# Kernel tuning notes

Hardware: AMD Instinct MI355X
Metric: run time of the kernel (lower is better)

## Reference

```python
import jax, jax.numpy as jnp
import numpy as np

NHEAD = 8
TOP_K = 2


def layernorm(x, g, b, eps=1e-5):
    m = x.mean(-1, keepdims=True)
    v = x.var(-1, keepdims=True)
    return (x - m) * jax.lax.rsqrt(v + eps) * g + b


def causal_conv(x, w, b, dil):
    # x: [N, C, L], w: [O, I, K] (torch layout), left-pad for causality
    pad = (w.shape[-1] - 1) * dil
    y = jax.lax.conv_general_dilated(x, w, (1,), [(pad, 0)], rhs_dilation=(dil,),
                                     dimension_numbers=('NCH', 'OIH', 'NCH'))
    return y + b[None, :, None]


def sinusoidal_pe(L, d):
    pos = jnp.arange(L, dtype=jnp.float32)[:, None]
    div = jnp.exp(jnp.arange(0, d, 2, dtype=jnp.float32) * (-np.log(10000.0) / d))
    pe = jnp.zeros((L, d), jnp.float32)
    pe = pe.at[:, 0::2].set(jnp.sin(pos * div))
    pe = pe.at[:, 1::2].set(jnp.cos(pos * div))
    return pe


def _forward(x, sensor_mask, enc_proj_w, enc_proj_b, tcn_w1, tcn_b1, tcn_w2, tcn_b2,
             enc_norm_g, enc_norm_b, pool_proj_w, pool_proj_b, pos_inter,
             t_wq, t_bq, t_wk, t_bk, t_wv, t_bv, t_wo, t_bo,
             t_ln1_g, t_ln1_b, t_ln2_g, t_ln2_b,
             t_ff1_w, t_ff1_b, t_ff2_w, t_ff2_b, t_out_g, t_out_b,
             exp_w1, exp_b1, exp_w2, exp_b2,
             gate_f_w, gate_f_b, gate_fail_w, gate_fail_b, gate_rca_w, gate_rca_b,
             pred_w, pred_b, fail_w, fail_b, rca_w, rca_b):
    B, L, M = x.shape
    P = enc_proj_w.shape[1]
    D = pool_proj_w.shape[1]
    O = exp_w2.shape[-1]
    # mask sensors, grab last value per sensor (globally standardized)
    xm = jnp.transpose(x, (0, 2, 1)) * sensor_mask[:, :, None]        # [B, M, L]
    last_val = xm[:, :, -1]                                           # [B, M]
    seqs = xm.reshape(B * M, L, 1)
    # per-sensor TCN encoder
    h = seqs @ enc_proj_w + enc_proj_b                                # [BM, L, P]
    h = h + sinusoidal_pe(L, P)[None]
    h = jnp.transpose(h, (0, 2, 1))                                   # [BM, P, L]
    for i in range(tcn_w1.shape[0]):
        dil = 2 ** i
        out = jax.nn.relu(causal_conv(h, tcn_w1[i], tcn_b1[i], dil))
        out = jax.nn.relu(causal_conv(out, tcn_w2[i], tcn_b2[i], dil))
        h = jax.nn.relu(out + h)                                      # channels equal -> identity residual
    h = layernorm(jnp.transpose(h, (0, 2, 1)), enc_norm_g, enc_norm_b)  # [BM, L, T]
    feats = h.reshape(B, M, L, -1) * sensor_mask[:, :, None, None]
    pooled = feats.mean(axis=2)                                       # [B, M, T]
    t = pooled @ pool_proj_w + pool_proj_b                            # [B, M, D]
    # inter-sensor transformer (pre-LN), key padding mask where sensor_mask==0
    t = t + pos_inter[:, :M, :]
    bias = jnp.where(sensor_mask == 0, -1e9, 0.0)[:, None, None, :]   # [B,1,1,M]
    dh = D // NHEAD
    for l in range(t_wq.shape[0]):
        y = layernorm(t, t_ln1_g[l], t_ln1_b[l])
        q = (y @ t_wq[l] + t_bq[l]).reshape(B, M, NHEAD, dh)
        k = (y @ t_wk[l] + t_bk[l]).reshape(B, M, NHEAD, dh)
        v = (y @ t_wv[l] + t_bv[l]).reshape(B, M, NHEAD, dh)
        s = jnp.einsum('bqhd,bkhd->bhqk', q, k) / jnp.sqrt(jnp.float32(dh)) + bias
        a = jax.nn.softmax(s, axis=-1)
        o = jnp.einsum('bhqk,bkhd->bqhd', a, v).reshape(B, M, D) @ t_wo[l] + t_bo[l]
        t = t + o
        y2 = layernorm(t, t_ln2_g[l], t_ln2_b[l])
        t = t + jax.nn.relu(y2 @ t_ff1_w[l] + t_ff1_b[l]) @ t_ff2_w[l] + t_ff2_b[l]
    ctx = layernorm(t, t_out_g, t_out_b) * sensor_mask[:, :, None]    # [B, M, D]
    # global context: masked mean + masked max over valid sensors
    cnt = jnp.maximum(sensor_mask.sum(1, keepdims=True), 1.0)
    mean_ctx = ctx.sum(1) / cnt                                       # [B, D]
    max_ctx = jnp.where(sensor_mask[:, :, None] > 0, ctx, -1e9).max(1)
    g = jnp.concatenate([mean_ctx, max_ctx], -1)                      # [B, 2D]

    def moe(x_exp, gate_in, gw, gb):
        logits = gate_in @ gw + gb                                    # [N, E]
        vals, idx = jax.lax.top_k(logits, TOP_K)
        w = jax.nn.softmax(vals, -1)
        hh = jax.nn.relu(jnp.einsum('nd,edh->neh', x_exp, exp_w1) + exp_b1)
        allo = jnp.einsum('neh,eho->neo', hh, exp_w2) + exp_b2        # [N, E, O]
        sel = jnp.take_along_axis(allo, idx[..., None], axis=1)
        return (sel * w[..., None]).sum(1)                            # [N, O]

    y_f = moe(g, g, gate_f_w, gate_f_b)                               # [B, O]
    y_fail = moe(g, g, gate_fail_w, gate_fail_b)
    tok = ctx.reshape(B * M, D)
    exp_in_rca = jnp.concatenate(
        [tok, jnp.broadcast_to(mean_ctx[:, None, :], (B, M, D)).reshape(B * M, D)], -1)
    y_rca = moe(exp_in_rca, tok, gate_rca_w, gate_rca_b).reshape(B, M, O)
    # heads
    pred_in = jnp.concatenate([pooled, ctx, jnp.broadcast_to(y_f[:, None, :], (B, M, O))], -1)
    pred = pred_in @ pred_w + pred_b + last_val[..., None]            # [B, M, PH]
    fail_out = y_fail @ fail_w + fail_b                               # [B, FH]
    rca_in = jnp.concatenate([pooled, ctx, y_rca], -1)
    rca_out = (rca_in @ rca_w + rca_b)[..., 0]                        # [B, M]
    return jnp.concatenate([pred.reshape(B, -1), fail_out, rca_out], axis=1)


def setup_inputs() -> dict:
    key = jax.random.key(0)
    ks = iter(jax.random.split(key, 64))
    nrm = lambda shape, s=0.05: jax.random.normal(next(ks), shape, jnp.float32) * s
    B, L, M = 16, 512, 32
    P, T, D, E, EH, O = 64, 64, 128, 16, 512, 128
    NL, LEV, K = 2, 4, 3
    return dict(
        x=jax.random.normal(next(ks), (B, L, M), jnp.float32),
        sensor_mask=jax.random.randint(next(ks), (B, M), 0, 2).astype(jnp.float32),
        enc_proj_w=nrm((1, P)), enc_proj_b=jnp.zeros((P,)),
        tcn_w1=nrm((LEV, P, P, K)), tcn_b1=jnp.zeros((LEV, P)),
        tcn_w2=nrm((LEV, P, P, K)), tcn_b2=jnp.zeros((LEV, P)),
        enc_norm_g=jnp.ones((T,)), enc_norm_b=jnp.zeros((T,)),
        pool_proj_w=nrm((T, D)), pool_proj_b=jnp.zeros((D,)),
        pos_inter=nrm((1, M, D), 0.02),
        t_wq=nrm((NL, D, D)), t_bq=jnp.zeros((NL, D)),
        t_wk=nrm((NL, D, D)), t_bk=jnp.zeros((NL, D)),
        t_wv=nrm((NL, D, D)), t_bv=jnp.zeros((NL, D)),
        t_wo=nrm((NL, D, D)), t_bo=jnp.zeros((NL, D)),
        t_ln1_g=jnp.ones((NL, D)), t_ln1_b=jnp.zeros((NL, D)),
        t_ln2_g=jnp.ones((NL, D)), t_ln2_b=jnp.zeros((NL, D)),
        t_ff1_w=nrm((NL, D, 2 * D)), t_ff1_b=jnp.zeros((NL, 2 * D)),
        t_ff2_w=nrm((NL, 2 * D, D)), t_ff2_b=jnp.zeros((NL, D)),
        t_out_g=jnp.ones((D,)), t_out_b=jnp.zeros((D,)),
        exp_w1=nrm((E, 2 * D, EH)), exp_b1=jnp.zeros((E, EH)),
        exp_w2=nrm((E, EH, O)), exp_b2=jnp.zeros((E, O)),
        gate_f_w=nrm((2 * D, E)), gate_f_b=jnp.zeros((E,)),
        gate_fail_w=nrm((2 * D, E)), gate_fail_b=jnp.zeros((E,)),
        gate_rca_w=nrm((D, E)), gate_rca_b=jnp.zeros((E,)),
        pred_w=nrm((T + D + O, 3)), pred_b=jnp.zeros((3,)),
        fail_w=nrm((O, 3)), fail_b=jnp.zeros((3,)),
        rca_w=nrm((T + D + O, 1)), rca_b=jnp.zeros((1,)),
    )


def reference(x, sensor_mask, enc_proj_w, enc_proj_b, tcn_w1, tcn_b1, tcn_w2, tcn_b2,
              enc_norm_g, enc_norm_b, pool_proj_w, pool_proj_b, pos_inter,
              t_wq, t_bq, t_wk, t_bk, t_wv, t_bv, t_wo, t_bo,
              t_ln1_g, t_ln1_b, t_ln2_g, t_ln2_b,
              t_ff1_w, t_ff1_b, t_ff2_w, t_ff2_b, t_out_g, t_out_b,
              exp_w1, exp_b1, exp_w2, exp_b2,
              gate_f_w, gate_f_b, gate_fail_w, gate_fail_b, gate_rca_w, gate_rca_b,
              pred_w, pred_b, fail_w, fail_b, rca_w, rca_b):
    return _forward(x, sensor_mask, enc_proj_w, enc_proj_b, tcn_w1, tcn_b1, tcn_w2, tcn_b2,
                    enc_norm_g, enc_norm_b, pool_proj_w, pool_proj_b, pos_inter,
                    t_wq, t_bq, t_wk, t_bk, t_wv, t_bv, t_wo, t_bo,
                    t_ln1_g, t_ln1_b, t_ln2_g, t_ln2_b,
                    t_ff1_w, t_ff1_b, t_ff2_w, t_ff2_b, t_out_g, t_out_b,
                    exp_w1, exp_b1, exp_w2, exp_b2,
                    gate_f_w, gate_f_b, gate_fail_w, gate_fail_b, gate_rca_w, gate_rca_b,
                    pred_w, pred_b, fail_w, fail_b, rca_w, rca_b)
```

## Files before the change

### kernel.cpp

```cpp
#include <hip/hip_runtime.h>
#include <hip/hip_bf16.h>

#define B_   16
#define L_   512
#define M_   32
#define P_   64
#define D_   128
#define NH_  8
#define NL_  2
#define E_   16
#define EH_  512
#define O_   128

#define CH2   256
#define HALO  60
#define PADF  16
#define ROWS2 336
#define LDW   64

typedef short  bf16x8 __attribute__((ext_vector_type(8)));
typedef float  f32x4  __attribute__((ext_vector_type(4)));
typedef unsigned short us4 __attribute__((ext_vector_type(4)));
typedef unsigned short us8 __attribute__((ext_vector_type(8)));

__device__ __forceinline__ float bf2f(unsigned short h) {
  unsigned u = ((unsigned)h) << 16; float f; __builtin_memcpy(&f, &u, 4); return f;
}
__device__ __forceinline__ unsigned short f2bf(float f) {
  unsigned u; __builtin_memcpy(&u, &f, 4);
  u += 0x7fffu + ((u >> 16) & 1);
  return (unsigned short)(u >> 16);
}
__device__ __forceinline__ int swz(int row, int col_us) {
  return row * LDW + (col_us ^ ((row & 7) << 3));
}

#define XFW_PPW   0
#define XFW_QKVO  8192
#define XFW_F1    139264
#define XFW_F2    204800

__global__ __launch_bounds__(256) void prep_kernel(
    const float* __restrict__ ppw,
    const float* __restrict__ twq, const float* __restrict__ twk,
    const float* __restrict__ twv, const float* __restrict__ two,
    const float* __restrict__ f1w, const float* __restrict__ f2w,
    const float* __restrict__ ew1, const float* __restrict__ ew2,
    const float* __restrict__ tw1, const float* __restrict__ tw2,
    unsigned short* __restrict__ xfw, unsigned short* __restrict__ w1t,
    unsigned short* __restrict__ w2t, unsigned short* __restrict__ wpack,
    float* __restrict__ peT) {
  const int b = blockIdx.x;
  const int tid = threadIdx.x;
  if (b < 834) {
    __shared__ float tl[64][65];
    const float* src; unsigned short* dst; int R, C, tr, tc;
    if (b < 2) {
      src = ppw; dst = xfw + XFW_PPW; R = 64; C = 128; tr = 0; tc = b;
    } else if (b < 34) {
      int t = b - 2; int lg = t >> 2; int l = lg >> 2, gem = lg & 3;
      int tt = t & 3; tr = tt >> 1; tc = tt & 1;
      const float* s4 = (gem == 0) ? twq : (gem == 1) ? twk : (gem == 2) ? twv : two;
      src = s4 + l * 16384; dst = xfw + XFW_QKVO + l * 65536 + gem * 16384; R = 128; C = 128;
    } else if (b < 50) {
      int t = b - 34; int l = t >> 3; int tt = t & 7; tr = tt >> 2; tc = tt & 3;
      src = f1w + l * 32768; dst = xfw + XFW_F1 + l * 32768; R = 128; C = 256;
    } else if (b < 66) {
      int t = b - 50; int l = t >> 3; int tt = t & 7; tr = tt >> 1; tc = tt & 1;
      src = f2w + l * 32768; dst = xfw + XFW_F2 + l * 32768; R = 256; C = 128;
    } else if (b < 578) {
      int t = b - 66; int e = t >> 5; int tt = t & 31; tr = tt >> 3; tc = tt & 7;
      src = ew1 + e * 131072; dst = w1t + e * 131072; R = 256; C = 512;
    } else {
      int t = b - 578; int e = t >> 4; int tt = t & 15; tr = tt >> 1; tc = tt & 1;
      src = ew2 + e * 65536; dst = w2t + e * 65536; R = 512; C = 128;
    }
    for (int i = tid; i < 4096; i += 256) {
      int r = i >> 6, c = i & 63;
      tl[r][c] = src[(tr * 64 + r) * C + tc * 64 + c];
    }
    __syncthreads();
    for (int i = tid; i < 4096; i += 256) {
      int c = i >> 6, r = i & 63;
      dst[(tc * 64 + c) * R + tr * 64 + r] = f2bf(tl[r][c]);
    }
  } else if (b < 840) {
    int base = (b - 834) * 16384;
    for (int q = tid; q < 16384; q += 256) {
      int i = base + q;
      int c = i & 63, o = (i >> 6) & 63, tlc = i >> 12;
      int t = tlc % 3, lc = tlc / 3, lvl = lc >> 1;
      const float* src = (lc & 1) ? tw2 : tw1;
      wpack[i] = f2bf(src[lvl * 12288 + o * 192 + c * 3 + t]);
    }
  } else {
    int base = (b - 840) * 16384;
    for (int q = tid; q < 16384; q += 256) {
      int j = base + q; int ll = j >> 6, c = j & 63;
      float dv = expf(-0.14391157f * (float)(c & ~1));
      float ang = (float)ll * dv;
      peT[j] = (c & 1) ? cosf(ang) : sinf(ang);
    }
  }
}

template <int DIL, bool RES>
__device__ __forceinline__ void conv_mfma(const unsigned short* __restrict__ IN,
                                          unsigned short* __restrict__ OUT,
                                          const unsigned short* __restrict__ Wt,
                                          const float* __restrict__ bias, bool zh) {
  const int tid  = threadIdx.x;
  const int wid  = tid >> 6;
  const int lane = tid & 63;
  const int fr   = lane & 15;
  const int g    = lane >> 4;
  const int ot0  = (wid & 1) * 2;
  const int ng   = wid >> 1;

  bf16x8 Af[2][6];
#pragma unroll
  for (int oo = 0; oo < 2; ++oo)
#pragma unroll
    for (int t = 0; t < 3; ++t)
#pragma unroll
      for (int kh = 0; kh < 2; ++kh) {
        int wr = t * 64 + (ot0 + oo) * 16 + fr;
        Af[oo][t * 2 + kh] = *(const bf16x8*)(Wt + swz(wr, kh * 32 + g * 8));
      }
  float bv[2][4];
#pragma unroll
  for (int oo = 0; oo < 2; ++oo)
#pragma unroll
    for (int j = 0; j < 4; ++j) bv[oo][j] = bias[(ot0 + oo) * 16 + g * 4 + j];

#pragma unroll
  for (int k = 0; k < 3; ++k) {
    const int nt = ng + k * 8;
    if (nt < 20) {
      const int rb = PADF + nt * 16 + fr;
      bf16x8 Bf[6];
#pragma unroll
      for (int t = 0; t < 3; ++t) {
        int r = rb + (t - 2) * DIL;
#pragma unroll
        for (int kh = 0; kh < 2; ++kh)
          Bf[t * 2 + kh] = *(const bf16x8*)(IN + swz(r, kh * 32 + g * 8));
      }
      f32x4 acc[2];
#pragma unroll
      for (int oo = 0; oo < 2; ++oo) {
        f32x4 a; a[0] = bv[oo][0]; a[1] = bv[oo][1]; a[2] = bv[oo][2]; a[3] = bv[oo][3];
        acc[oo] = a;
      }
#pragma unroll
      for (int f = 0; f < 6; ++f)
#pragma unroll
        for (int oo = 0; oo < 2; ++oo)
          acc[oo] = __builtin_amdgcn_mfma_f32_16x16x32_bf16(Af[oo][f], Bf[f], acc[oo], 0, 0, 0);

      const float zm = (zh && rb < PADF + HALO) ? 0.f : 1.f;
#pragma unroll
      for (int oo = 0; oo < 2; ++oo) {
        unsigned short* op = OUT + swz(rb, (ot0 + oo) * 16 + g * 4);
        us4 old;
        if (RES) old = *(const us4*)op;
        us4 st;
#pragma unroll
        for (int j = 0; j < 4; ++j) {
          float v = fmaxf(acc[oo][j], 0.f);
          if (RES) v = fmaxf(v + bf2f(old[j]), 0.f);
          st[j] = f2bf(v * zm);
        }
        *(us4*)op = st;
      }
    }
  }
}

__global__ __launch_bounds__(1024) void tcn_kernel(
    const float* __restrict__ x, const float* __restrict__ mask,
    const float* __restrict__ pw, const float* __restrict__ pb,
    const unsigned short* __restrict__ wpack,
    const float* __restrict__ b1, const float* __restrict__ b2,
    const float* __restrict__ peT,
    const float* __restrict__ lng, const float* __restrict__ lnb,
    float* __restrict__ psum2) {
  extern __shared__ unsigned short smu[];
  unsigned short* A  = smu;
  unsigned short* Bq = A + ROWS2 * LDW;
  unsigned short* W0 = Bq + ROWS2 * LDW;
  unsigned short* W1 = W0 + 192 * LDW;
  float* fbase = (float*)(W1 + 192 * LDW);
  float* xr   = fbase;
  float* pwpb = fbase + 336;
  float* mst  = fbase;
  float* pp   = fbase + 512;

  const int bx = blockIdx.x;
  const int seq = bx & 511;
  const int chunk = bx >> 9;
  const int b = seq >> 5;
  const int m = seq & 31;
  if (mask[b * M_ + m] == 0.0f) return;
  const int tid = threadIdx.x;
  const bool zh = (chunk == 0);
  const int lbase = chunk * CH2 - HALO;

  float4 wreg[2];
#define WLOAD(li)                                                               \
  { wreg[0] = *(const float4*)(wpack + (li) * 12288 + (tid >> 3) * 64 + (tid & 7) * 8); \
    if (tid < 512)                                                              \
      wreg[1] = *(const float4*)(wpack + (li) * 12288 + ((tid >> 3) + 128) * 64 + (tid & 7) * 8); }
#define WSTORE(buf)                                                             \
  { *(float4*)((buf) + swz(tid >> 3, (tid & 7) * 8)) = wreg[0];                 \
    if (tid < 512)                                                              \
      *(float4*)((buf) + swz((tid >> 3) + 128, (tid & 7) * 8)) = wreg[1]; }

  WLOAD(0);
  if (tid < 64)       pwpb[tid] = pw[tid];
  else if (tid < 128) pwpb[tid] = pb[tid - 64];
  if (tid < ROWS2) {
    int w = tid - PADF, l = lbase + w;
    float xv = 0.f;
    if (w >= 0 && w < CH2 + HALO && l >= 0 && l < L_) xv = x[(b * L_ + l) * M_ + m];
    xr[tid] = xv;
  }
  __syncthreads();

  for (int idx = tid; idx < ROWS2 * 8; idx += 1024) {
    int r = idx >> 3, c0 = (idx & 7) * 8;
    int w = r - PADF, l = lbase + w;
    us8 st;
    if (w >= 0 && w < CH2 + HALO && l >= 0 && l < L_) {
      float xv = xr[r];
      const float4* pe4 = (const float4*)(peT + l * 64 + c0);
      float4 pa = pe4[0], pc = pe4[1];
      float pe[8] = {pa.x, pa.y, pa.z, pa.w, pc.x, pc.y, pc.z, pc.w};
#pragma unroll
      for (int j = 0; j < 8; ++j) {
        int c = c0 + j;
        st[j] = f2bf(fmaf(xv, pwpb[c], pwpb[64 + c]) + pe[j]);
      }
    } else {
#pragma unroll
      for (int j = 0; j < 8; ++j) st[j] = 0;
    }
    *(us8*)(A + swz(r, c0)) = st;
  }
  for (int idx = tid; idx < PADF * LDW; idx += 1024) Bq[idx] = 0;
  WSTORE(W0); WLOAD(1);
  __syncthreads();

  conv_mfma<1, false>(A, Bq, W0, b1 + 0,   zh); WSTORE(W1); WLOAD(2); __syncthreads();
  conv_mfma<1, true >(Bq, A, W1, b2 + 0,   zh); WSTORE(W0); WLOAD(3); __syncthreads();
  conv_mfma<2, false>(A, Bq, W0, b1 + 64,  zh); WSTORE(W1); WLOAD(4); __syncthreads();
  conv_mfma<2, true >(Bq, A, W1, b2 + 64,  zh); WSTORE(W0); WLOAD(5); __syncthreads();
  conv_mfma<4, false>(A, Bq, W0, b1 + 128, zh); WSTORE(W1); WLOAD(6); __syncthreads();
  conv_mfma<4, true >(Bq, A, W1, b2 + 128, zh); WSTORE(W0); WLOAD(7); __syncthreads();
  conv_mfma<8, false>(A, Bq, W0, b1 + 192, zh); WSTORE(W1);           __syncthreads();
  conv_mfma<8, true >(Bq, A, W1, b2 + 192, zh);                       __syncthreads();
#undef WLOAD
#undef WSTORE

  if (tid < CH2) {
    int r = PADF + HALO + tid;
    float s = 0.f, ss = 0.f;
#pragma unroll
    for (int c0 = 0; c0 < 64; c0 += 8) {
      bf16x8 vv = *(const bf16x8*)(A + swz(r, c0));
#pragma unroll
      for (int j = 0; j < 8; ++j) { float v = bf2f((unsigned short)vv[j]); s += v; ss += v * v; }
    }
    float mu = s * 0.015625f;
    float var = fmaxf(ss * 0.015625f - mu * mu, 0.0f);
    mst[tid] = mu;
    mst[CH2 + tid] = rsqrtf(var + 1e-5f);
  }
  __syncthreads();
  {
    int p = tid & 63, q = tid >> 6;
    float accp = 0.f;
    int r0 = PADF + HALO + q * 16;
    for (int r = r0; r < r0 + 16; ++r)
      accp += (bf2f(A[swz(r, p)]) - mst[r - PADF - HALO]) * mst[CH2 + r - PADF - HALO];
    pp[tid] = accp;
  }
  __syncthreads();
  if (tid < 64) {
    float acc = 0.f;
#pragma unroll
    for (int q = 0; q < 16; ++q) acc += pp[q * 64 + tid];
    psum2[chunk * 32768 + seq * 64 + tid] = lng[tid] * acc + 256.0f * lnb[tid];
  }
}

__global__ __launch_bounds__(1024) void xf_kernel(
    const float* __restrict__ psum2, const float* __restrict__ mask,
    const unsigned short* __restrict__ xfw,
    const float* __restrict__ ppb, const float* __restrict__ pos,
    const float* __restrict__ bq, const float* __restrict__ bk,
    const float* __restrict__ bv, const float* __restrict__ bo,
    const float* __restrict__ l1g, const float* __restrict__ l1b,
    const float* __restrict__ l2g, const float* __restrict__ l2b,
    const float* __restrict__ f1b, const float* __restrict__ f2b,
    const float* __restrict__ og_, const float* __restrict__ ob_,
    const float* __restrict__ gfw, const float* __restrict__ gfb,
    const float* __restrict__ glw, const float* __restrict__ glb,
    const float* __restrict__ grw, const float* __restrict__ grb,
    float* __restrict__ pooledws, float* __restrict__ ctxws,
    float* __restrict__ gwt, int* __restrict__ ecnt, int* __restrict__ elist,
    unsigned short* __restrict__ xbf) {
  extern __shared__ float sm[];
  float* T    = sm;
  float* QKV  = T + 4224;
  float* S    = QKV + 12672;
  float* gv   = S + 8448;
  float* mkv  = gv + 512;
  unsigned short* Ybf = (unsigned short*)(mkv + 64);
  unsigned short* Yb2 = Ybf + 32 * 136;
  unsigned short* FFH = Yb2 + 32 * 136;
  const int b = blockIdx.x;
  const int tid = threadIdx.x;
  const int wid = tid >> 6;
  const int lane = tid & 63;
  const int fr = lane & 15;
  const int g = lane >> 4;
  const int row32 = tid >> 5;
  const int ln32  = tid & 31;

  if (tid < 32) mkv[tid] = mask[b * 32 + tid];
  for (int idx = tid; idx < 2048; idx += 1024) {
    int mm = idx >> 6, p = idx & 63;
    const float* p4 = psum2 + (b * 32 + mm) * 64 + p;
    float v = (p4[0] + p4[32768]) * mask[b * 32 + mm] * (1.0f / 512.0f);
    pooledws[(b * 32 + mm) * 64 + p] = v;
    Ybf[mm * 136 + p] = f2bf(v);
  }
  __syncthreads();

  {
    int mt = wid >> 3, nt = wid & 7;
    bf16x8 Af[2];
#pragma unroll
    for (int kf = 0; kf < 2; ++kf)
      Af[kf] = *(const bf16x8*)(Ybf + (mt * 16 + fr) * 136 + kf * 32 + g * 8);
    const unsigned short* bp = xfw + XFW_PPW + (nt * 16 + fr) * 64;
    f32x4 acc = {0.f, 0.f, 0.f, 0.f};
#pragma unroll
    for (int kf = 0; kf < 2; ++kf)
      acc = __builtin_amdgcn_mfma_f32_16x16x32_bf16(Af[kf], *(const bf16x8*)(bp + kf * 32 + g * 8), acc, 0, 0, 0);
    int n = nt * 16 + fr;
    float bb = ppb[n];
#pragma unroll
    for (int j = 0; j < 4; ++j) {
      int m = mt * 16 + g * 4 + j;
      T[m * 132 + n] = acc[j] + bb + pos[m * 128 + n];
    }
  }
  __syncthreads();

#define LN_BF(GAMMA, BETA)                                                     \
  {                                                                            \
    int mm = row32, j0 = ln32 * 4;                                             \
    float4 v4 = *(const float4*)(T + mm * 132 + j0);                           \
    float s = v4.x + v4.y + v4.z + v4.w;                                       \
    float ss = v4.x * v4.x + v4.y * v4.y + v4.z * v4.z + v4.w * v4.w;          \
    _Pragma("unroll") for (int mk = 16; mk >= 1; mk >>= 1) {                   \
      s += __shfl_xor(s, mk); ss += __shfl_xor(ss, mk);                        \
    }                                                                          \
    float mu = s * 0.0078125f;                                                 \
    float rstd = rsqrtf(fmaxf(ss * 0.0078125f - mu * mu, 0.f) + 1e-5f);        \
    us4 st;                                                                    \
    float vv[4] = {v4.x, v4.y, v4.z, v4.w};                                    \
    _Pragma("unroll") for (int j = 0; j < 4; ++j)                              \
      st[j] = f2bf((vv[j] - mu) * rstd * (GAMMA)[j0 + j] + (BETA)[j0 + j]);    \
    *(us4*)(Ybf + mm * 136 + j0) = st;                                         \
  }                                                                            \
  __syncthreads();

  for (int l = 0; l < NL_; ++l) {
    LN_BF(l1g + l * 128, l1b + l * 128)
#pragma unroll
    for (int i = 0; i < 3; ++i) {
      int tt = wid * 3 + i;
      int gem = tt >> 4, r = tt & 15, mt = r >> 3, nt = r & 7;
      const unsigned short* wT = xfw + XFW_QKVO + l * 65536 + gem * 16384;
      const float* bias = (gem == 0) ? bq : (gem == 1) ? bk : bv;
      bf16x8 Afr[4];
#pragma unroll
      for (int kf = 0; kf < 4; ++kf)
        Afr[kf] = *(const bf16x8*)(Ybf + (mt * 16 + fr) * 136 + kf * 32 + g * 8);
      const unsigned short* bp = wT + (nt * 16 + fr) * 128;
      f32x4 acc = {0.f, 0.f, 0.f, 0.f};
#pragma unroll
      for (int kf = 0; kf < 4; ++kf)
        acc = __builtin_amdgcn_mfma_f32_16x16x32_bf16(Afr[kf], *(const bf16x8*)(bp + kf * 32 + g * 8), acc, 0, 0, 0);
      int n = nt * 16 + fr;
      float bb = bias[l * 128 + n];
#pragma unroll
      for (int j = 0; j < 4; ++j)
        QKV[(mt * 16 + g * 4 + j) * 396 + gem * 132 + n] = acc[j] + bb;
    }
    __syncthreads();

    {
      int n = ln32;
      float mbias = (mkv[n] == 0.0f) ? -1e9f : 0.f;
#pragma unroll
      for (int t = 0; t < 8; ++t) {
        int task = row32 * 8 + t;
        int h = task >> 5, mm = task & 31;
        const float* qp = QKV + mm * 396 + h * 16;
        const float* kp = QKV + n * 396 + 132 + h * 16;
        float a = 0;
#pragma unroll
        for (int d = 0; d < 16; ++d) a = fmaf(qp[d], kp[d], a);
        a = a * 0.25f + mbias;
        float mx = a;
#pragma unroll
        for (int mk = 16; mk >= 1; mk >>= 1) mx = fmaxf(mx, __shfl_xor(mx, mk));
        float e = __expf(a - mx);
        float sum = e;
#pragma unroll
        for (int mk = 16; mk >= 1; mk >>= 1) sum += __shfl_xor(sum, mk);
        S[h * 1056 + mm * 33 + n] = e / sum;
      }
    }
    __syncthreads();

    {
      int mm = row32, j0 = ln32 * 4, h = j0 >> 4;
      const float* sp = S + h * 1056 + mm * 33;
      f32x4 a = {0.f, 0.f, 0.f, 0.f};
#pragma unroll 8
      for (int n = 0; n < 32; ++n) {
        float p = sp[n];
        float4 v4 = *(const float4*)(QKV + n * 396 + 264 + j0);
        a[0] = fmaf(p, v4.x, a[0]); a[1] = fmaf(p, v4.y, a[1]);
        a[2] = fmaf(p, v4.z, a[2]); a[3] = fmaf(p, v4.w, a[3]);
      }
      us4 st;
#pragma unroll
      for (int j = 0; j < 4; ++j) st[j] = f2bf(a[j]);
      *(us4*)(Yb2 + mm * 136 + j0) = st;
    }
    __syncthreads();

    {
      int mt = wid >> 3, nt = wid & 7;
      bf16x8 Aw[4];
#pragma unroll
      for (int kf = 0; kf < 4; ++kf)
        Aw[kf] = *(const bf16x8*)(Yb2 + (mt * 16 + fr) * 136 + kf * 32 + g * 8);
      const unsigned short* bp = xfw + XFW_QKVO + l * 65536 + 3 * 16384 + (nt * 16 + fr) * 128;
      f32x4 acc = {0.f, 0.f, 0.f, 0.f};
#pragma unroll
      for (int kf = 0; kf < 4; ++kf)
        acc = __builtin_amdgcn_mfma_f32_16x16x32_bf16(Aw[kf], *(const bf16x8*)(bp + kf * 32 + g * 8), acc, 0, 0, 0);
      int n = nt * 16 + fr;
      float bb = bo[l * 128 + n];
#pragma unroll
      for (int j = 0; j < 4; ++j)
        T[(mt * 16 + g * 4 + j) * 132 + n] += acc[j] + bb;
    }
    __syncthreads();

    LN_BF(l2g + l * 128, l2b + l * 128)
#pragma unroll
    for (int i = 0; i < 2; ++i) {
      int tt = wid * 2 + i;
      int mt = tt >> 4, nt = tt & 15;
      bf16x8 Aff[4];
#pragma unroll
      for (int kf = 0; kf < 4; ++kf)
        Aff[kf] = *(const bf16x8*)(Ybf + (mt * 16 + fr) * 136 + kf * 32 + g * 8);
      const unsigned short* bp = xfw + XFW_F1 + l * 32768 + (nt * 16 + fr) * 128;
      f32x4 acc = {0.f, 0.f, 0.f, 0.f};
#pragma unroll
      for (int kf = 0; kf < 4; ++kf)
        acc = __builtin_amdgcn_mfma_f32_16x16x32_bf16(Aff[kf], *(const bf16x8*)(bp + kf * 32 + g * 8), acc, 0, 0, 0);
      int n = nt * 16 + fr;
      float bb = f1b[l * 256 + n];
#pragma unroll
      for (int j = 0; j < 4; ++j)
        FFH[(mt * 16 + g * 4 + j) * 264 + n] = f2bf(fmaxf(acc[j] + bb, 0.f));
    }
    __syncthreads();
    {
      int mt = wid >> 3, nt = wid & 7;
      bf16x8 Af2[8];
#pragma unroll
      for (int kf = 0; kf < 8; ++kf)
        Af2[kf] = *(const bf16x8*)(FFH + (mt * 16 + fr) * 264 + kf * 32 + g * 8);
      const unsigned short* bp = xfw + XFW_F2 + l * 32768 + (nt * 16 + fr) * 256;
      f32x4 acc = {0.f, 0.f, 0.f, 0.f};
#pragma unroll
      for (int kf = 0; kf < 8; ++kf)
        acc = __builtin_amdgcn_mfma_f32_16x16x32_bf16(Af2[kf], *(const bf16x8*)(bp + kf * 32 + g * 8), acc, 0, 0, 0);
      int n = nt * 16 + fr;
      float bb = f2b[l * 128 + n];
#pragma unroll
      for (int j = 0; j < 4; ++j)
        T[(mt * 16 + g * 4 + j) * 132 + n] += acc[j] + bb;
    }
    __syncthreads();
  }
#undef LN_BF

  {
    int mm = row32, j0 = ln32 * 4;
    float4 v4 = *(const float4*)(T + mm * 132 + j0);
    float s = v4.x + v4.y + v4.z + v4.w;
    float ss = v4.x * v4.x + v4.y * v4.y + v4.z * v4.z + v4.w * v4.w;
#pragma unroll
    for (int mk = 16; mk >= 1; mk >>= 1) { s += __shfl_xor(s, mk); ss += __shfl_xor(ss, mk); }
    float mu = s * 0.0078125f;
    float rstd = rsqrtf(fmaxf(ss * 0.0078125f - mu * mu, 0.f) + 1e-5f);
    float mk_ = mkv[mm];
    float vv[4] = {v4.x, v4.y, v4.z, v4.w};
#pragma unroll
    for (int j = 0; j < 4; ++j) {
      float c = ((vv[j] - mu) * rstd * og_[j0 + j] + ob_[j0 + j]) * mk_;
      S[mm * 132 + j0 + j] = c;
      ctxws[(b * 32 + mm) * 128 + j0 + j] = c;
    }
  }
  __syncthreads();
  if (tid < 128) {
    float cnt = 0;
    for (int mm = 0; mm < 32; ++mm) cnt += mkv[mm];
    cnt = fmaxf(cnt, 1.0f);
    float s = 0, mx = -1e9f;
    for (int mm = 0; mm < 32; ++mm) {
      float v = S[mm * 132 + tid];
      s += v;
      if (mkv[mm] > 0.0f) mx = fmaxf(mx, v);
    }
    gv[tid] = s / cnt;
    gv[128 + tid] = mx;
  }
  __syncthreads();

  float* lg = QKV;
  if (tid < 544) {
    int lr = tid >> 4, e = tid & 15;
    float a;
    if (lr == 0) {
      a = gfb[e];
      for (int d = 0; d < 256; ++d) a = fmaf(gv[d], gfw[d * 16 + e], a);
    } else if (lr == 1) {
      a = glb[e];
      for (int d = 0; d < 256; ++d) a = fmaf(gv[d], glw[d * 16 + e], a);
    } else {
      int mm = lr - 2;
      a = grb[e];
      for (int d = 0; d < 128; ++d) a = fmaf(S[mm * 132 + d], grw[d * 16 + e], a);
    }
    lg[lr * 16 + e] = a;
  }
  __syncthreads();
  if (tid < 34) {
    const float* lgr = lg + tid * 16;
    int i0 = 0; float v0 = lgr[0];
    for (int e = 1; e < 16; ++e) if (lgr[e] > v0) { v0 = lgr[e]; i0 = e; }
    int i1 = (i0 == 0) ? 1 : 0; float v1 = lgr[i1];
    for (int e = 0; e < 16; ++e) if (e != i0 && lgr[e] > v1) { v1 = lgr[e]; i1 = e; }
    float e1 = __expf(v1 - v0);
    float w0 = 1.0f / (1.0f + e1);
    int gr = (tid == 0) ? b : (tid == 1) ? (16 + b) : (32 + b * 32 + (tid - 2));
    gwt[2 * gr] = w0;  gwt[2 * gr + 1] = 1.0f - w0;
    int p0 = atomicAdd(&ecnt[i0], 1); elist[i0 * 544 + p0] = 2 * gr;
    int p1 = atomicAdd(&ecnt[i1], 1); elist[i1 * 544 + p1] = 2 * gr + 1;
  }
  for (int j = tid; j < 34 * 256; j += 1024) {
    int lr = j >> 8, d = j & 255;
    float v;
    if (lr < 2) v = gv[d];
    else        v = (d < 128) ? S[(lr - 2) * 132 + d] : gv[d - 128];
    int gr = (lr == 0) ? b : (lr == 1) ? (16 + b) : (32 + b * 32 + (lr - 2));
    xbf[gr * 256 + d] = f2bf(v);
  }
}

__global__ __launch_bounds__(512) void moe_kernel(
    const unsigned short* __restrict__ xbf, const float* __restrict__ gwt,
    const int* __restrict__ elist, const int* __restrict__ ecnt,
    const unsigned short* __restrict__ w1t, const float* __restrict__ eb1,
    const unsigned short* __restrict__ w2t, const float* __restrict__ eb2,
    float* __restrict__ yall) {
  __shared__ unsigned short Xb[16 * 264];
  __shared__ unsigned short Hb[16 * 520];
  __shared__ float wl[16];
  __shared__ int rowl[16];
  const int e = blockIdx.x >> 3;
  const int slot = blockIdx.x & 7;
  const int n = ecnt[e];
  const int ntiles = (n + 15) >> 4;
  const int tid = threadIdx.x;
  const int wid = tid >> 6;
  const int lane = tid & 63;
  const int fr = lane & 15;
  const int g = lane >> 4;

  for (int t = slot; t < ntiles; t += 8) {
    if (tid < 16) {
      int idx = t * 16 + tid;
      int id = (idx < n) ? elist[e * 544 + idx] : -1;
      rowl[tid] = (id >= 0) ? (id >> 1) : -1;
      wl[tid] = (id >= 0) ? gwt[id] : 0.f;
    }
    __syncthreads();
    for (int i = tid; i < 512; i += 512) {
      int r = i >> 5, c8 = (i & 31) * 8;
      int row = rowl[r];
      bf16x8 v = {0, 0, 0, 0, 0, 0, 0, 0};
      if (row >= 0) v = *(const bf16x8*)(xbf + row * 256 + c8);
      *(bf16x8*)(Xb + r * 264 + c8) = v;
    }
    __syncthreads();
    bf16x8 Af[8];
#pragma unroll
    for (int kf = 0; kf < 8; ++kf)
      Af[kf] = *(const bf16x8*)(Xb + fr * 264 + kf * 32 + g * 8);
#pragma unroll
    for (int ntl = 0; ntl < 4; ++ntl) {
      int nt = wid * 4 + ntl;
      const unsigned short* bp = w1t + (e * 512 + nt * 16 + fr) * 256;
      f32x4 acc = {0.f, 0.f, 0.f, 0.f};
#pragma unroll
      for (int kf = 0; kf < 8; ++kf)
        acc = __builtin_amdgcn_mfma_f32_16x16x32_bf16(Af[kf], *(const bf16x8*)(bp + kf * 32 + g * 8), acc, 0, 0, 0);
      int h = nt * 16 + fr;
      float b1v = eb1[e * 512 + h];
#pragma unroll
      for (int j = 0; j < 4; ++j)
        Hb[(g * 4 + j) * 520 + h] = f2bf(fmaxf(acc[j] + b1v, 0.f));
    }
    __syncthreads();
    {
      const unsigned short* bp = w2t + (e * 128 + wid * 16 + fr) * 512;
      f32x4 acc = {0.f, 0.f, 0.f, 0.f};
#pragma unroll
      for (int kf = 0; kf < 16; ++kf) {
        bf16x8 Ah = *(const bf16x8*)(Hb + fr * 520 + kf * 32 + g * 8);
        acc = __builtin_amdgcn_mfma_f32_16x16x32_bf16(Ah, *(const bf16x8*)(bp + kf * 32 + g * 8), acc, 0, 0, 0);
      }
      int o = wid * 16 + fr;
      float b2v = eb2[e * 128 + o];
#pragma unroll
      for (int j = 0; j < 4; ++j) {
        int r = g * 4 + j;
        int row = rowl[r];
        if (row >= 0) atomicAdd(&yall[row * 128 + o], wl[r] * (acc[j] + b2v));
      }
    }
    __syncthreads();
  }
}

__global__ __launch_bounds__(192) void heads_kernel(
    const float* __restrict__ x, const float* __restrict__ mask,
    const float* __restrict__ pooledws, const float* __restrict__ ctxws,
    const float* __restrict__ yf, const float* __restrict__ yfail, const float* __restrict__ yrca,
    const float* __restrict__ pw, const float* __restrict__ pb,
    const float* __restrict__ fw, const float* __restrict__ fb,
    const float* __restrict__ rw, const float* __restrict__ rb,
    float* __restrict__ out) {
  __shared__ float yfb[128];
  int b = blockIdx.x, t = threadIdx.x;
  if (t < 128) yfb[t] = yf[b * 128 + t];
  __syncthreads();
  if (t < 96) {
    int mm = t / 3, o = t - mm * 3;
    int s = b * 32 + mm;
    float a = pb[o];
    const float* pl = pooledws + s * 64;
    for (int i = 0; i < 64; ++i) a = fmaf(pl[i], pw[i * 3 + o], a);
    const float* cx = ctxws + s * 128;
    for (int i = 0; i < 128; ++i) a = fmaf(cx[i], pw[(64 + i) * 3 + o], a);
    for (int i = 0; i < 128; ++i) a = fmaf(yfb[i], pw[(192 + i) * 3 + o], a);
    a += x[(b * 512 + 511) * 32 + mm] * mask[b * 32 + mm];
    out[b * 131 + t] = a;
  } else if (t < 99) {
    int o = t - 96;
    float a = fb[o];
    const float* yl = yfail + b * 128;
    for (int i = 0; i < 128; ++i) a = fmaf(yl[i], fw[i * 3 + o], a);
    out[b * 131 + 96 + o] = a;
  } else if (t < 131) {
    int mm = t - 99;
    int s = b * 32 + mm;
    float a = rb[0];
    const float* pl = pooledws + s * 64;
    for (int i = 0; i < 64; ++i) a = fmaf(pl[i], rw[i], a);
    const float* cx = ctxws + s * 128;
    for (int i = 0; i < 128; ++i) a = fmaf(cx[i], rw[64 + i], a);
    const float* yr = yrca + s * 128;
    for (int i = 0; i < 128; ++i) a = fmaf(yr[i], rw[192 + i], a);
    out[b * 131 + 99 + mm] = a;
  }
}

extern "C" void kernel_launch(void* const* d_in, const int* in_sizes, int n_in,
                              void* d_out, int out_size, void* d_ws, size_t ws_size,
                              hipStream_t stream) {
  (void)in_sizes; (void)n_in; (void)out_size; (void)ws_size;
  const float* x    = (const float*)d_in[0];
  const float* msk  = (const float*)d_in[1];
  const float* epw  = (const float*)d_in[2];
  const float* epb  = (const float*)d_in[3];
  const float* tw1  = (const float*)d_in[4];
  const float* tb1  = (const float*)d_in[5];
  const float* tw2  = (const float*)d_in[6];
  const float* tb2  = (const float*)d_in[7];
  const float* eng  = (const float*)d_in[8];
  const float* enb  = (const float*)d_in[9];
  const float* ppw  = (const float*)d_in[10];
  const float* ppb  = (const float*)d_in[11];
  const float* pos  = (const float*)d_in[12];
  const float* twq  = (const float*)d_in[13];
  const float* tbq  = (const float*)d_in[14];
  const float* twk  = (const float*)d_in[15];
  const float* tbk  = (const float*)d_in[16];
  const float* twv  = (const float*)d_in[17];
  const float* tbv  = (const float*)d_in[18];
  const float* two  = (const float*)d_in[19];
  const float* tbo  = (const float*)d_in[20];
  const float* l1g  = (const float*)d_in[21];
  const float* l1b  = (const float*)d_in[22];
  const float* l2g  = (const float*)d_in[23];
  const float* l2b  = (const float*)d_in[24];
  const float* f1w  = (const float*)d_in[25];
  const float* f1b  = (const float*)d_in[26];
  const float* f2w  = (const float*)d_in[27];
  const float* f2b  = (const float*)d_in[28];
  const float* tog  = (const float*)d_in[29];
  const float* tob  = (const float*)d_in[30];
  const float* ew1  = (const float*)d_in[31];
  const float* eb1  = (const float*)d_in[32];
  const float* ew2  = (const float*)d_in[33];
  const float* eb2  = (const float*)d_in[34];
  const float* gfw  = (const float*)d_in[35];
  const float* gfb  = (const float*)d_in[36];
  const float* glw  = (const float*)d_in[37];
  const float* glb  = (const float*)d_in[38];
  const float* grw  = (const float*)d_in[39];
  const float* grb  = (const float*)d_in[40];
  const float* prw  = (const float*)d_in[41];
  const float* prb  = (const float*)d_in[42];
  const float* fw   = (const float*)d_in[43];
  const float* fb   = (const float*)d_in[44];
  const float* rw   = (const float*)d_in[45];
  const float* rb   = (const float*)d_in[46];

  float* ws      = (float*)d_ws;
  float* psum2   = ws;
  float* pooledw = psum2 + 65536;
  float* ctxw    = pooledw + 32768;
  float* yall    = ctxw + 65536;
  float* gwt     = yall + 69632;
  int*   ecnt    = (int*)(gwt + 1088);
  int*   elist   = ecnt + 16;
  float* peT     = (float*)(elist + 8704);
  unsigned short* wpack = (unsigned short*)(peT + 32768);
  unsigned short* xfw   = wpack + 98304;
  unsigned short* w1t   = xfw + 270336;
  unsigned short* w2t   = w1t + 2097152;
  unsigned short* xbf   = w2t + 1048576;

  const int tcn_lds = (2 * ROWS2 * LDW + 2 * 192 * LDW) * 2 + 1536 * 4;
  const int xf_lds  = (4224 + 12672 + 8448 + 512 + 64) * 4 + (2 * 4352 + 8448) * 2;
  hipFuncSetAttribute((const void*)tcn_kernel, hipFuncAttributeMaxDynamicSharedMemorySize, tcn_lds);
  hipFuncSetAttribute((const void*)xf_kernel,  hipFuncAttributeMaxDynamicSharedMemorySize, xf_lds);

  hipMemsetAsync(yall, 0, 69632 * sizeof(float), stream);
  hipMemsetAsync(ecnt, 0, 16 * sizeof(int), stream);

  prep_kernel<<<842, 256, 0, stream>>>(ppw, twq, twk, twv, two, f1w, f2w, ew1, ew2,
                                       tw1, tw2, xfw, w1t, w2t, wpack, peT);
  tcn_kernel<<<1024, 1024, tcn_lds, stream>>>(x, msk, epw, epb, wpack, tb1, tb2, peT,
                                              eng, enb, psum2);
  xf_kernel<<<16, 1024, xf_lds, stream>>>(psum2, msk, xfw, ppb, pos,
                                          tbq, tbk, tbv, tbo,
                                          l1g, l1b, l2g, l2b, f1b, f2b,
                                          tog, tob,
                                          gfw, gfb, glw, glb, grw, grb,
                                          pooledw, ctxw, gwt, ecnt, elist, xbf);
  moe_kernel<<<128, 512, 0, stream>>>(xbf, gwt, elist, ecnt, w1t, eb1, w2t, eb2, yall);
  heads_kernel<<<16, 192, 0, stream>>>(x, msk, pooledw, ctxw,
                                       yall, yall + 2048, yall + 4096,
                                       prw, prb, fw, fb, rw, rb, (float*)d_out);
}
```

Measured before the change: 241.8 us.

## Process full sequence per block and read conv weights directly from global

The TCN kernel now handles each sensor's whole 512-step sequence in one block, replacing two overlapping 256-step chunks with a 60-row halo. This removes the recomputed halo rows and the half-block of idle row tiles, and the partial-sum merge in the transformer kernel goes away. Conv weights are loaded into registers straight from global memory (L2-cached) instead of being staged through double-buffered LDS, which frees LDS and removes the staging stores. In exchange, the grid halves to 512 blocks, so there is less parallelism across the GPU, and each wave makes global weight loads on every layer.

```diff
diff --git a/kernel.cpp b/kernel.cpp
--- a/kernel.cpp
+++ b/kernel.cpp
@@ -12,10 +12,8 @@
 #define EH_  512
 #define O_   128
 
-#define CH2   256
-#define HALO  60
 #define PADF  16
-#define ROWS2 336
+#define ROWSF 528
 #define LDW   64
 
 typedef short  bf16x8 __attribute__((ext_vector_type(8)));
@@ -105,10 +103,10 @@
 }
 
 template <int DIL, bool RES>
-__device__ __forceinline__ void conv_mfma(const unsigned short* __restrict__ IN,
-                                          unsigned short* __restrict__ OUT,
-                                          const unsigned short* __restrict__ Wt,
-                                          const float* __restrict__ bias, bool zh) {
+__device__ __forceinline__ void conv_gw(const unsigned short* __restrict__ IN,
+                                        unsigned short* __restrict__ OUT,
+                                        const unsigned short* __restrict__ wp,
+                                        const float* __restrict__ bias) {
   const int tid  = threadIdx.x;
   const int wid  = tid >> 6;
   const int lane = tid & 63;
@@ -123,56 +121,51 @@
 #pragma unroll
     for (int t = 0; t < 3; ++t)
 #pragma unroll
-      for (int kh = 0; kh < 2; ++kh) {
-        int wr = t * 64 + (ot0 + oo) * 16 + fr;
-        Af[oo][t * 2 + kh] = *(const bf16x8*)(Wt + swz(wr, kh * 32 + g * 8));
+      for (int kh = 0; kh < 2; ++kh)
+        Af[oo][t * 2 + kh] =
+            *(const bf16x8*)(wp + (t * 64 + (ot0 + oo) * 16 + fr) * 64 + kh * 32 + g * 8);
+  float bv[2][4];
+#pragma unroll
+  for (int oo = 0; oo < 2; ++oo)
+#pragma unroll
+    for (int j = 0; j < 4; ++j) bv[oo][j] = bias[(ot0 + oo) * 16 + g * 4 + j];
+
+#pragma unroll
+  for (int k = 0; k < 4; ++k) {
+    const int rb = PADF + (ng + k * 8) * 16 + fr;
+    bf16x8 Bf[6];
+#pragma unroll
+    for (int t = 0; t < 3; ++t) {
+      int r = rb + (t - 2) * DIL;
+#pragma unroll
+      for (int kh = 0; kh < 2; ++kh)
+        Bf[t * 2 + kh] = *(const bf16x8*)(IN + swz(r, kh * 32 + g * 8));
+    }
+    f32x4 acc[2];
+#pragma unroll
+    for (int oo = 0; oo < 2; ++oo) {
+      f32x4 a; a[0] = bv[oo][0]; a[1] = bv[oo][1]; a[2] = bv[oo][2]; a[3] = bv[oo][3];
+      acc[oo] = a;
+    }
+#pragma unroll
+    for (int f = 0; f < 6; ++f)
+#pragma unroll
+      for (int oo = 0; oo < 2; ++oo)
+        acc[oo] = __builtin_amdgcn_mfma_f32_16x16x32_bf16(Af[oo][f], Bf[f], acc[oo], 0, 0, 0);
+
+#pragma unroll
+    for (int oo = 0; oo < 2; ++oo) {
+      unsigned short* op = OUT + swz(rb, (ot0 + oo) * 16 + g * 4);
+      us4 old;
+      if (RES) old = *(const us4*)op;
+      us4 st;
+#pragma unroll
+      for (int j = 0; j < 4; ++j) {
+        float v = fmaxf(acc[oo][j], 0.f);
+        if (RES) v = fmaxf(v + bf2f(old[j]), 0.f);
+        st[j] = f2bf(v);
       }
-  float bv[2][4];
-#pragma unroll
-  for (int oo = 0; oo < 2; ++oo)
-#pragma unroll
-    for (int j = 0; j < 4; ++j) bv[oo][j] = bias[(ot0 + oo) * 16 + g * 4 + j];
-
-#pragma unroll
-  for (int k = 0; k < 3; ++k) {
-    const int nt = ng + k * 8;
-    if (nt < 20) {
-      const int rb = PADF + nt * 16 + fr;
-      bf16x8 Bf[6];
-#pragma unroll
-      for (int t = 0; t < 3; ++t) {
-        int r = rb + (t - 2) * DIL;
-#pragma unroll
-        for (int kh = 0; kh < 2; ++kh)
-          Bf[t * 2 + kh] = *(const bf16x8*)(IN + swz(r, kh * 32 + g * 8));
-      }
-      f32x4 acc[2];
-#pragma unroll
-      for (int oo = 0; oo < 2; ++oo) {
-        f32x4 a; a[0] = bv[oo][0]; a[1] = bv[oo][1]; a[2] = bv[oo][2]; a[3] = bv[oo][3];
-        acc[oo] = a;
-      }
-#pragma unroll
-      for (int f = 0; f < 6; ++f)
-#pragma unroll
-        for (int oo = 0; oo < 2; ++oo)
-          acc[oo] = __builtin_amdgcn_mfma_f32_16x16x32_bf16(Af[oo][f], Bf[f], acc[oo], 0, 0, 0);
-
-      const float zm = (zh && rb < PADF + HALO) ? 0.f : 1.f;
-#pragma unroll
-      for (int oo = 0; oo < 2; ++oo) {
-        unsigned short* op = OUT + swz(rb, (ot0 + oo) * 16 + g * 4);
-        us4 old;
-        if (RES) old = *(const us4*)op;
-        us4 st;
-#pragma unroll
-        for (int j = 0; j < 4; ++j) {
-          float v = fmaxf(acc[oo][j], 0.f);
-          if (RES) v = fmaxf(v + bf2f(old[j]), 0.f);
-          st[j] = f2bf(v * zm);
-        }
-        *(us4*)op = st;
-      }
+      *(us4*)op = st;
     }
   }
 }
@@ -184,86 +177,64 @@
     const float* __restrict__ b1, const float* __restrict__ b2,
     const float* __restrict__ peT,
     const float* __restrict__ lng, const float* __restrict__ lnb,
-    float* __restrict__ psum2) {
+    float* __restrict__ psum) {
   extern __shared__ unsigned short smu[];
   unsigned short* A  = smu;
-  unsigned short* Bq = A + ROWS2 * LDW;
-  unsigned short* W0 = Bq + ROWS2 * LDW;
-  unsigned short* W1 = W0 + 192 * LDW;
-  float* fbase = (float*)(W1 + 192 * LDW);
-  float* xr   = fbase;
-  float* pwpb = fbase + 336;
-  float* mst  = fbase;
-  float* pp   = fbase + 512;
-
-  const int bx = blockIdx.x;
-  const int seq = bx & 511;
-  const int chunk = bx >> 9;
+  unsigned short* Bq = A + ROWSF * LDW;
+  float* pwpb = (float*)(Bq + ROWSF * LDW);
+  float* mst  = pwpb + 128;
+  float* pp   = mst + 1024;
+
+  const int seq = blockIdx.x;
   const int b = seq >> 5;
   const int m = seq & 31;
   if (mask[b * M_ + m] == 0.0f) return;
   const int tid = threadIdx.x;
-  const bool zh = (chunk == 0);
-  const int lbase = chunk * CH2 - HALO;
-
-  float4 wreg[2];
-#define WLOAD(li)                                                               \
-  { wreg[0] = *(const float4*)(wpack + (li) * 12288 + (tid >> 3) * 64 + (tid & 7) * 8); \
-    if (tid < 512)                                                              \
-      wreg[1] = *(const float4*)(wpack + (li) * 12288 + ((tid >> 3) + 128) * 64 + (tid & 7) * 8); }
-#define WSTORE(buf)                                                             \
-  { *(float4*)((buf) + swz(tid >> 3, (tid & 7) * 8)) = wreg[0];                 \
-    if (tid < 512)                                                              \
-      *(float4*)((buf) + swz((tid >> 3) + 128, (tid & 7) * 8)) = wreg[1]; }
-
-  WLOAD(0);
-  if (tid < 64)       pwpb[tid] = pw[tid];
-  else if (tid < 128) pwpb[tid] = pb[tid - 64];
-  if (tid < ROWS2) {
-    int w = tid - PADF, l = lbase + w;
-    float xv = 0.f;
-    if (w >= 0 && w < CH2 + HALO && l >= 0 && l < L_) xv = x[(b * L_ + l) * M_ + m];
-    xr[tid] = xv;
-  }
-  __syncthreads();
-
-  for (int idx = tid; idx < ROWS2 * 8; idx += 1024) {
-    int r = idx >> 3, c0 = (idx & 7) * 8;
-    int w = r - PADF, l = lbase + w;
-    us8 st;
-    if (w >= 0 && w < CH2 + HALO && l >= 0 && l < L_) {
-      float xv = xr[r];
-      const float4* pe4 = (const float4*)(peT + l * 64 + c0);
-      float4 pa = pe4[0], pc = pe4[1];
-      float pe[8] = {pa.x, pa.y, pa.z, pa.w, pc.x, pc.y, pc.z, pc.w};
-#pragma unroll
-      for (int j = 0; j < 8; ++j) {
-        int c = c0 + j;
-        st[j] = f2bf(fmaf(xv, pwpb[c], pwpb[64 + c]) + pe[j]);
+
+  if (tid < 64)        pwpb[tid] = pw[tid];
+  else if (tid < 128)  pwpb[tid] = pb[tid - 64];
+  __syncthreads();
+
+  if (tid < ROWSF) {
+    int r = tid;
+    if (r >= PADF) {
+      int l = r - PADF;
+      float xv = x[(b * L_ + l) * M_ + m];
+      const float4* pe4 = (const float4*)(peT + l * 64);
+#pragma unroll
+      for (int c0 = 0; c0 < 64; c0 += 8) {
+        float4 pa = pe4[c0 / 4], pc = pe4[c0 / 4 + 1];
+        float pe[8] = {pa.x, pa.y, pa.z, pa.w, pc.x, pc.y, pc.z, pc.w};
+        us8 st;
+#pragma unroll
+        for (int j = 0; j < 8; ++j) {
+          int c = c0 + j;
+          st[j] = f2bf(fmaf(xv, pwpb[c], pwpb[64 + c]) + pe[j]);
+        }
+        *(us8*)(A + swz(r, c0)) = st;
       }
     } else {
-#pragma unroll
-      for (int j = 0; j < 8; ++j) st[j] = 0;
-    }
-    *(us8*)(A + swz(r, c0)) = st;
-  }
-  for (int idx = tid; idx < PADF * LDW; idx += 1024) Bq[idx] = 0;
-  WSTORE(W0); WLOAD(1);
-  __syncthreads();
-
-  conv_mfma<1, false>(A, Bq, W0, b1 + 0,   zh); WSTORE(W1); WLOAD(2); __syncthreads();
-  conv_mfma<1, true >(Bq, A, W1, b2 + 0,   zh); WSTORE(W0); WLOAD(3); __syncthreads();
-  conv_mfma<2, false>(A, Bq, W0, b1 + 64,  zh); WSTORE(W1); WLOAD(4); __syncthreads();
-  conv_mfma<2, true >(Bq, A, W1, b2 + 64,  zh); WSTORE(W0); WLOAD(5); __syncthreads();
-  conv_mfma<4, false>(A, Bq, W0, b1 + 128, zh); WSTORE(W1); WLOAD(6); __syncthreads();
-  conv_mfma<4, true >(Bq, A, W1, b2 + 128, zh); WSTORE(W0); WLOAD(7); __syncthreads();
-  conv_mfma<8, false>(A, Bq, W0, b1 + 192, zh); WSTORE(W1);           __syncthreads();
-  conv_mfma<8, true >(Bq, A, W1, b2 + 192, zh);                       __syncthreads();
-#undef WLOAD
-#undef WSTORE
-
-  if (tid < CH2) {
-    int r = PADF + HALO + tid;
+      us8 z = {0, 0, 0, 0, 0, 0, 0, 0};
+#pragma unroll
+      for (int c0 = 0; c0 < 64; c0 += 8) {
+        *(us8*)(A + swz(r, c0)) = z;
+        *(us8*)(Bq + swz(r, c0)) = z;
+      }
+    }
+  }
+  __syncthreads();
+
+  conv_gw<1, false>(A, Bq, wpack + 0 * 12288, b1 + 0);   __syncthreads();
+  conv_gw<1, true >(Bq, A, wpack + 1 * 12288, b2 + 0);   __syncthreads();
+  conv_gw<2, false>(A, Bq, wpack + 2 * 12288, b1 + 64);  __syncthreads();
+  conv_gw<2, true >(Bq, A, wpack + 3 * 12288, b2 + 64);  __syncthreads();
+  conv_gw<4, false>(A, Bq, wpack + 4 * 12288, b1 + 128); __syncthreads();
+  conv_gw<4, true >(Bq, A, wpack + 5 * 12288, b2 + 128); __syncthreads();
+  conv_gw<8, false>(A, Bq, wpack + 6 * 12288, b1 + 192); __syncthreads();
+  conv_gw<8, true >(Bq, A, wpack + 7 * 12288, b2 + 192); __syncthreads();
+
+  if (tid < 512) {
+    int r = PADF + tid;
     float s = 0.f, ss = 0.f;
 #pragma unroll
     for (int c0 = 0; c0 < 64; c0 += 8) {
@@ -274,15 +245,15 @@
     float mu = s * 0.015625f;
     float var = fmaxf(ss * 0.015625f - mu * mu, 0.0f);
     mst[tid] = mu;
-    mst[CH2 + tid] = rsqrtf(var + 1e-5f);
+    mst[512 + tid] = rsqrtf(var + 1e-5f);
   }
   __syncthreads();
   {
     int p = tid & 63, q = tid >> 6;
     float accp = 0.f;
-    int r0 = PADF + HALO + q * 16;
-    for (int r = r0; r < r0 + 16; ++r)
-      accp += (bf2f(A[swz(r, p)]) - mst[r - PADF - HALO]) * mst[CH2 + r - PADF - HALO];
+    int r0 = PADF + q * 32;
+    for (int r = r0; r < r0 + 32; ++r)
+      accp += (bf2f(A[swz(r, p)]) - mst[r - PADF]) * mst[512 + r - PADF];
     pp[tid] = accp;
   }
   __syncthreads();
@@ -290,12 +261,12 @@
     float acc = 0.f;
 #pragma unroll
     for (int q = 0; q < 16; ++q) acc += pp[q * 64 + tid];
-    psum2[chunk * 32768 + seq * 64 + tid] = lng[tid] * acc + 256.0f * lnb[tid];
+    psum[seq * 64 + tid] = lng[tid] * acc + 512.0f * lnb[tid];
   }
 }
 
 __global__ __launch_bounds__(1024) void xf_kernel(
-    const float* __restrict__ psum2, const float* __restrict__ mask,
+    const float* __restrict__ psum, const float* __restrict__ mask,
     const unsigned short* __restrict__ xfw,
     const float* __restrict__ ppb, const float* __restrict__ pos,
     const float* __restrict__ bq, const float* __restrict__ bk,
@@ -331,8 +302,7 @@
   if (tid < 32) mkv[tid] = mask[b * 32 + tid];
   for (int idx = tid; idx < 2048; idx += 1024) {
     int mm = idx >> 6, p = idx & 63;
-    const float* p4 = psum2 + (b * 32 + mm) * 64 + p;
-    float v = (p4[0] + p4[32768]) * mask[b * 32 + mm] * (1.0f / 512.0f);
+    float v = psum[(b * 32 + mm) * 64 + p] * mask[b * 32 + mm] * (1.0f / 512.0f);
     pooledws[(b * 32 + mm) * 64 + p] = v;
     Ybf[mm * 136 + p] = f2bf(v);
   }
@@ -754,8 +724,8 @@
   const float* rb   = (const float*)d_in[46];
 
   float* ws      = (float*)d_ws;
-  float* psum2   = ws;
-  float* pooledw = psum2 + 65536;
+  float* psum    = ws;
+  float* pooledw = psum + 32768;
   float* ctxw    = pooledw + 32768;
   float* yall    = ctxw + 65536;
   float* gwt     = yall + 69632;
@@ -768,7 +738,7 @@
   unsigned short* w2t   = w1t + 2097152;
   unsigned short* xbf   = w2t + 1048576;
 
-  const int tcn_lds = (2 * ROWS2 * LDW + 2 * 192 * LDW) * 2 + 1536 * 4;
+  const int tcn_lds = 2 * ROWSF * LDW * 2 + (128 + 1024 + 1024) * 4;
   const int xf_lds  = (4224 + 12672 + 8448 + 512 + 64) * 4 + (2 * 4352 + 8448) * 2;
   hipFuncSetAttribute((const void*)tcn_kernel, hipFuncAttributeMaxDynamicSharedMemorySize, tcn_lds);
   hipFuncSetAttribute((const void*)xf_kernel,  hipFuncAttributeMaxDynamicSharedMemorySize, xf_lds);
@@ -778,9 +748,9 @@
 
   prep_kernel<<<842, 256, 0, stream>>>(ppw, twq, twk, twv, two, f1w, f2w, ew1, ew2,
                                        tw1, tw2, xfw, w1t, w2t, wpack, peT);
-  tcn_kernel<<<1024, 1024, tcn_lds, stream>>>(x, msk, epw, epb, wpack, tb1, tb2, peT,
-                                              eng, enb, psum2);
-  xf_kernel<<<16, 1024, xf_lds, stream>>>(psum2, msk, xfw, ppb, pos,
+  tcn_kernel<<<512, 1024, tcn_lds, stream>>>(x, msk, epw, epb, wpack, tb1, tb2, peT,
+                                             eng, enb, psum);
+  xf_kernel<<<16, 1024, xf_lds, stream>>>(psum, msk, xfw, ppb, pos,
                                           tbq, tbk, tbv, tbo,
                                           l1g, l1b, l2g, l2b, f1b, f2b,
                                           tog, tob,
```

Result: slower. 290.2 us (+20.0%).
